# Kernel optimization log

Hardware: AMD Instinct MI355X
Metric: run time of the kernel (lower is better)

## Reference

```python
import jax, jax.numpy as jnp
import numpy as np

METRIC = (1.0, 1.0, 1.0, 1.0, -1.0)  # Cl(4,1) signature
N_HEADS = 8
EPS = 1e-6


def _cayley():
    # Cayley table C[a, b, k]: e_a * e_b = sum_k C[a,b,k] e_k, blades indexed by bitmask over 5 generators.
    C = np.zeros((32, 32, 32), dtype=np.float32)
    for a in range(32):
        for b in range(32):
            s = 0
            t = a >> 1
            while t:
                s += bin(t & b).count('1')
                t >>= 1
            sign = -1.0 if (s & 1) else 1.0
            for i in range(5):
                if (a & b) >> i & 1:
                    sign *= METRIC[i]
            C[a, b, a ^ b] = sign
    return C

_C_NP = _cayley()
GP_MAP = jnp.asarray(_C_NP)  # (32,32,32)
SIG = jnp.asarray(_C_NP[np.arange(32), np.arange(32), 0])  # blade square signs, (32,)


def normalize_cl41(x):
    # normalize each multivector (last-dim 32 blades) to unit RMS
    return x / jnp.sqrt(jnp.mean(x * x, axis=-1, keepdims=True) + EPS)


def versor_linear(x, W):
    # x: (B,S,I,32), W: (O,I,32); out_k = sum_{i,j,l} W[o,i,j] C[j,l,k] x[b,s,i,l]
    O, I, _ = W.shape
    W_op = jnp.einsum('oij,jlk->oilk', W, GP_MAP)  # (O,I,32,32)
    W_mat = W_op.transpose(1, 2, 0, 3).reshape(I * 32, O * 32)
    B, S = x.shape[0], x.shape[1]
    out = (x.reshape(B, S, I * 32) @ W_mat).reshape(B, S, O, 32)
    return normalize_cl41(out)


def versor_attention(x, Wq, Wk, Wv, Wo, lam):
    B, S, D, _ = x.shape
    H = N_HEADS
    hd = D // H

    def split_heads(t):  # (B,S,D,32) -> (B,H,S,hd,32)
        return t.reshape(B, S, H, hd, 32).transpose(0, 2, 1, 3, 4)

    q = split_heads(versor_linear(x, Wq))
    k = split_heads(versor_linear(x, Wk))
    v = split_heads(versor_linear(x, Wv))

    q_flat = (q * SIG).reshape(B, H, S, hd * 32)  # signature-weighted
    k_flat = k.reshape(B, H, S, hd * 32)

    scalar = jnp.einsum('bhsd,bhtd->bhst', q_flat, k_flat)
    scale = 1.0 / jnp.sqrt(jnp.asarray(hd, x.dtype))
    score = scalar * scale

    # torque term: sqrt(relu(|q|^2 |k|^2 - (q.k)^2) + eps) / sqrt(hd)
    q_norm_sq = jnp.sum(q_flat * q_flat, axis=-1)[..., :, None]  # (B,H,S,1)
    k_norm_sq = jnp.sum(k_flat * k_flat, axis=-1)[..., None, :]  # (B,H,1,S)
    torque = jnp.sqrt(jax.nn.relu(q_norm_sq * k_norm_sq - scalar * scalar) + EPS) * scale
    score = score + lam * torque

    probs = jax.nn.softmax(score, axis=-1)
    out = jnp.einsum('bhst,bhtdl->bhsdl', probs, v)  # (B,H,S,hd,32)
    out = out.transpose(0, 2, 1, 3, 4).reshape(B, S, D, 32)
    return versor_linear(out, Wo)


def setup_inputs() -> dict:
    key = jax.random.key(0)
    ks = jax.random.split(key, 5)
    B, S, D = 2, 1024, 128
    std = (2.0 / (D * 32)) ** 0.5  # Versor init
    x = jax.random.normal(ks[0], (B, S, D, 32), jnp.float32)
    Wq = jax.random.normal(ks[1], (D, D, 32), jnp.float32) * std
    Wk = jax.random.normal(ks[2], (D, D, 32), jnp.float32) * std
    Wv = jax.random.normal(ks[3], (D, D, 32), jnp.float32) * std
    Wo = jax.random.normal(ks[4], (D, D, 32), jnp.float32) * std
    attn_lambda = jnp.float32(0.1)
    return {'x': x, 'Wq': Wq, 'Wk': Wk, 'Wv': Wv, 'Wo': Wo, 'attn_lambda': attn_lambda}


def reference(x, Wq, Wk, Wv, Wo, attn_lambda):
    return versor_attention(x, Wq, Wk, Wv, Wo, attn_lambda)
```

## Files before the change

kernel.cpp:

```cpp
#include <hip/hip_runtime.h>
#include <stdint.h>

typedef __attribute__((ext_vector_type(4))) float    f32x4;
typedef __attribute__((ext_vector_type(8))) short    s16x8;
typedef __attribute__((ext_vector_type(4))) short    s16x4;
typedef __attribute__((ext_vector_type(8))) _Float16 f16x8;

#define DEV __device__ __forceinline__

DEV float blade_sign(int a, int b){
    int s = 0, t = a >> 1;
    while (t){ s += __popc(t & b); t >>= 1; }
    float sg = (s & 1) ? -1.0f : 1.0f;
    return ((a & b) & 16) ? -sg : sg;
}
DEV short f2h(float v){
    _Float16 h = (_Float16)v;
    return __builtin_bit_cast(short, h);
}
DEV float h2f(short b){
    return (float)__builtin_bit_cast(_Float16, b);
}
DEV void wait_vm(int n){
    if (n == 12)     asm volatile("s_waitcnt vmcnt(12)" ::: "memory");
    else if (n == 8) asm volatile("s_waitcnt vmcnt(8)" ::: "memory");
    else if (n == 6) asm volatile("s_waitcnt vmcnt(6)" ::: "memory");
    else if (n == 4) asm volatile("s_waitcnt vmcnt(4)" ::: "memory");
    else             asm volatile("s_waitcnt vmcnt(0)" ::: "memory");
}

__global__ __launch_bounds__(256) void cast_f32_f16(const float* __restrict__ in,
                                                    short* __restrict__ out){
    const size_t idx = (size_t)blockIdx.x * 256 + threadIdx.x;
    const float4* p = reinterpret_cast<const float4*>(in) + idx * 2;
    float4 a = p[0], b = p[1];
    s16x8 o;
    o[0]=f2h(a.x); o[1]=f2h(a.y); o[2]=f2h(a.z); o[3]=f2h(a.w);
    o[4]=f2h(b.x); o[5]=f2h(b.y); o[6]=f2h(b.z); o[7]=f2h(b.w);
    *reinterpret_cast<s16x8*>(out + idx * 8) = o;
}

DEV void build_wmat_body(const float* __restrict__ W, short* __restrict__ WmT,
                         int idx){
    const int n  = idx >> 9;
    const int kg = idx & 511;
    const int o = n >> 5, kb = n & 31;
    const int i = kg >> 2, l0 = (kg & 3) * 8;
    const float* wrow = W + (size_t)(o * 128 + i) * 32;
    s16x8 v;
    #pragma unroll
    for (int e = 0; e < 8; ++e){
        const int l = l0 + e, j = kb ^ l;
        v[e] = f2h(wrow[j] * blade_sign(j, l));
    }
    *reinterpret_cast<s16x8*>(WmT + (size_t)n * 4096 + kg * 8) = v;
}

__global__ __launch_bounds__(256) void build_wmat(const float* __restrict__ W,
                                                  short* __restrict__ WmT){
    build_wmat_body(W, WmT, blockIdx.x * 256 + threadIdx.x);
}

__global__ __launch_bounds__(256) void build_wmat3(const float* __restrict__ Wq,
                                                   const float* __restrict__ Wk,
                                                   const float* __restrict__ Wv,
                                                   short* __restrict__ WmT3){
    const int w = blockIdx.y;
    const float* W = (w == 0) ? Wq : ((w == 1) ? Wk : Wv);
    build_wmat_body(W, WmT3 + (size_t)w * 4096 * 4096,
                    blockIdx.x * 256 + threadIdx.x);
}

__global__ __launch_bounds__(256) void row_norms(const short* __restrict__ Q,
                                                 const short* __restrict__ Kq,
                                                 float* __restrict__ Nq,
                                                 float* __restrict__ Nk){
    const int row  = blockIdx.x * 4 + (threadIdx.x >> 6);
    const int lane = threadIdx.x & 63;
    const int b = row >> 13, h = (row >> 10) & 7, s = row & 1023;
    const size_t off = ((size_t)(b * 1024 + s)) * 4096 + h * 512 + lane * 8;
    s16x8 a = *reinterpret_cast<const s16x8*>(Q + off);
    s16x8 c = *reinterpret_cast<const s16x8*>(Kq + off);
    float sq = 0.f, sk = 0.f;
    #pragma unroll
    for (int e = 0; e < 8; ++e){
        float fa = h2f(a[e]); sq = fmaf(fa, fa, sq);
        float fc = h2f(c[e]); sk = fmaf(fc, fc, sk);
    }
    #pragma unroll
    for (int m = 1; m < 64; m <<= 1){
        sq += __shfl_xor(sq, m);
        sk += __shfl_xor(sk, m);
    }
    if (lane == 0){ Nq[row] = sq; Nk[row] = sk; }
}

__global__ __launch_bounds__(256) void softmax_rows(float* __restrict__ Sc){
    const int row  = blockIdx.x * 4 + (threadIdx.x >> 6);
    const int lane = threadIdx.x & 63;
    float* p = Sc + (size_t)row * 1024;
    float v[16];
    float mx = -3.0e38f;
    #pragma unroll
    for (int j = 0; j < 16; ++j){ v[j] = p[lane + j * 64]; mx = fmaxf(mx, v[j]); }
    #pragma unroll
    for (int m = 1; m < 64; m <<= 1) mx = fmaxf(mx, __shfl_xor(mx, m));
    float sum = 0.f;
    #pragma unroll
    for (int j = 0; j < 16; ++j){ v[j] = __expf(v[j] - mx); sum += v[j]; }
    #pragma unroll
    for (int m = 1; m < 64; m <<= 1) sum += __shfl_xor(sum, m);
    const float inv = 1.0f / sum;
    short* pb = reinterpret_cast<short*>(p);
    #pragma unroll
    for (int j = 0; j < 16; ++j) pb[lane + j * 64] = f2h(v[j] * inv);
}

#define GLOAD_LDS(gp, lp) \
    __builtin_amdgcn_global_load_lds( \
        (const __attribute__((address_space(1))) void*)(const void*)(gp), \
        (__attribute__((address_space(3))) void*)(void*)(lp), 16, 0, 0)

#define QKV_TILE(T, WN, PF)                                                     \
  {                                                                             \
    const int bb = cur * 12288;                                                 \
    wait_vm(WN);                                                                \
    __builtin_amdgcn_s_barrier();                                               \
    asm volatile("" ::: "memory");                                              \
    __builtin_amdgcn_sched_barrier(0);                                          \
    const int sb = stg * 12288;                                                 \
    if (PF){                                                                    \
        GLOAD_LDS(gA0 + (size_t)((T) + 2) * 32, lds + sb + dA + 0 * 512);       \
        GLOAD_LDS(gA1 + (size_t)((T) + 2) * 32, lds + sb + dA + 1 * 512);       \
        GLOAD_LDS(gA2 + (size_t)((T) + 2) * 32, lds + sb + dA + 2 * 512);       \
        GLOAD_LDS(gA3 + (size_t)((T) + 2) * 32, lds + sb + dA + 3 * 512);       \
    }                                                                           \
    f16x8 av[4], bv[4];                                                         \
    _Pragma("unroll")                                                           \
    for (int i = 0; i < 4; ++i){                                                \
        av[i] = *reinterpret_cast<const f16x8*>(lds + bb + ard + i * 512);      \
        bv[i] = *reinterpret_cast<const f16x8*>(lds + bb + brd + i * 512);      \
    }                                                                           \
    __builtin_amdgcn_s_setprio(1);                                              \
    _Pragma("unroll")                                                           \
    for (int mi = 0; mi < 4; ++mi)                                              \
        _Pragma("unroll")                                                       \
        for (int ni = 0; ni < 4; ++ni)                                          \
            acc[mi][ni] = __builtin_amdgcn_mfma_f32_16x16x32_f16(               \
                av[mi], bv[ni], acc[mi][ni], 0, 0, 0);                          \
    __builtin_amdgcn_s_setprio(0);                                              \
    if (PF){                                                                    \
        GLOAD_LDS(gB0 + (size_t)((T) + 2) * 32, lds + sb + dB + 0 * 512);       \
        GLOAD_LDS(gB1 + (size_t)((T) + 2) * 32, lds + sb + dB + 1 * 512);       \
    }                                                                           \
    f16x8 aw[4];                                                                \
    _Pragma("unroll")                                                           \
    for (int i = 0; i < 4; ++i)                                                 \
        aw[i] = *reinterpret_cast<const f16x8*>(lds + bb + ard + (4 + i) * 512);\
    __builtin_amdgcn_s_setprio(1);                                              \
    _Pragma("unroll")                                                           \
    for (int mi = 0; mi < 4; ++mi)                                              \
        _Pragma("unroll")                                                       \
        for (int ni = 0; ni < 4; ++ni)                                          \
            acc[4 + mi][ni] = __builtin_amdgcn_mfma_f32_16x16x32_f16(           \
                aw[mi], bv[ni], acc[4 + mi][ni], 0, 0, 0);                      \
    __builtin_amdgcn_s_setprio(0);                                              \
    cur = (cur == 2) ? 0 : cur + 1;                                             \
    stg = (stg == 2) ? 0 : stg + 1;                                             \
  }

__global__ __launch_bounds__(256, 2) void versor_gemm_qkv2(
    const short* __restrict__ Xf,
    const short* __restrict__ WmT3,
    short* __restrict__ OQ,
    short* __restrict__ OK,
    short* __restrict__ OV)
{
    extern __shared__ short lds[];

    const int tid  = threadIdx.x;
    const int lane = tid & 63;
    const int wid  = tid >> 6;
    const int wm   = wid >> 1;
    const int wn   = wid & 1;

    const int wg  = blockIdx.x + blockIdx.y * 96;
    const int xcd = wg & 7;
    const int u   = wg >> 3;
    const int bm  = u & 7;
    const int bn  = xcd * 12 + (u >> 3);
    const int row0 = bm * 256;
    const int col0 = bn * 128;

    const int lda = 4096, ldb = 4096;

    const int jsw = ((lane & 3) ^ ((lane >> 3) & 3)) * 8;
    const short* gA0 = Xf + (size_t)(row0 + wid * 64 + (lane >> 2)) * lda + jsw;
    const short* gA1 = gA0 + (size_t)16 * lda;
    const short* gA2 = gA0 + (size_t)32 * lda;
    const short* gA3 = gA0 + (size_t)48 * lda;
    const short* gB0 = WmT3 + (size_t)(col0 + wid * 32 + (lane >> 2)) * ldb + jsw;
    const short* gB1 = gB0 + (size_t)16 * ldb;
    const int dA = wid * 4 * 512;
    const int dB = 8192 + wid * 2 * 512;

    const int swz = ((lane >> 4) ^ (((lane & 15) >> 1) & 3)) * 8;
    const int ard = (wm * 128 + (lane & 15)) * 32 + swz;
    const int brd = 8192 + (wn * 64 + (lane & 15)) * 32 + swz;

    f32x4 acc[8][4];
    #pragma unroll
    for (int i = 0; i < 8; ++i)
        #pragma unroll
        for (int j = 0; j < 4; ++j)
            acc[i][j] = (f32x4){0.f, 0.f, 0.f, 0.f};

    const int NT = 4096 >> 5;

    #pragma unroll
    for (int pt = 0; pt < 2; ++pt){
        const int sb = pt * 12288;
        GLOAD_LDS(gA0 + pt * 32, lds + sb + dA + 0 * 512);
        GLOAD_LDS(gA1 + pt * 32, lds + sb + dA + 1 * 512);
        GLOAD_LDS(gA2 + pt * 32, lds + sb + dA + 2 * 512);
        GLOAD_LDS(gA3 + pt * 32, lds + sb + dA + 3 * 512);
        GLOAD_LDS(gB0 + pt * 32, lds + sb + dB + 0 * 512);
        GLOAD_LDS(gB1 + pt * 32, lds + sb + dB + 1 * 512);
    }

    int cur = 0, stg = 2;
    for (int t = 0; t < NT - 1; ++t)
        QKV_TILE(t, 6, (t + 2 < NT))
    QKV_TILE(NT - 1, 0, false)

    const int rb = row0 + wm * 128 + (lane >> 4) * 4;

    #pragma unroll
    for (int mi = 0; mi < 8; ++mi){
        #pragma unroll
        for (int g = 0; g < 2; ++g){
            f32x4 a0 = acc[mi][2 * g], a1 = acc[mi][2 * g + 1];
            f32x4 ss = a0 * a0 + a1 * a1;
            #pragma unroll
            for (int m = 1; m < 16; m <<= 1){
                ss.x += __shfl_xor(ss.x, m);
                ss.y += __shfl_xor(ss.y, m);
                ss.z += __shfl_xor(ss.z, m);
                ss.w += __shfl_xor(ss.w, m);
            }
            f32x4 inv;
            inv.x = 1.0f / sqrtf(ss.x * 0.03125f + 1e-6f);
            inv.y = 1.0f / sqrtf(ss.y * 0.03125f + 1e-6f);
            inv.z = 1.0f / sqrtf(ss.z * 0.03125f + 1e-6f);
            inv.w = 1.0f / sqrtf(ss.w * 0.03125f + 1e-6f);
            acc[mi][2 * g]     = a0 * inv;
            acc[mi][2 * g + 1] = a1 * inv;
        }
    }

    const int zsel = col0 >> 12;
    const int cbm  = (col0 & 4095) + wn * 64 + (lane & 15);
    if (zsel == 0){
        const float sg0 = blade_sign(lane & 15, lane & 15);
        const float sg1 = blade_sign(16 | (lane & 15), 16 | (lane & 15));
        #pragma unroll
        for (int mi = 0; mi < 8; ++mi)
            #pragma unroll
            for (int ni = 0; ni < 4; ++ni){
                const f32x4 v = acc[mi][ni] * ((ni & 1) ? sg1 : sg0);
                #pragma unroll
                for (int j = 0; j < 4; ++j)
                    OQ[(size_t)(rb + mi * 16 + j) * 4096 + (cbm + ni * 16)] = f2h(v[j]);
            }
    } else if (zsel == 1){
        #pragma unroll
        for (int mi = 0; mi < 8; ++mi)
            #pragma unroll
            for (int ni = 0; ni < 4; ++ni)
                #pragma unroll
                for (int j = 0; j < 4; ++j)
                    OK[(size_t)(rb + mi * 16 + j) * 4096 + (cbm + ni * 16)] = f2h(acc[mi][ni][j]);
    } else {
        #pragma unroll
        for (int mi = 0; mi < 8; ++mi){
            const int r = rb + mi * 16;
            const int b = r >> 10, tt = r & 1023;
            #pragma unroll
            for (int ni = 0; ni < 4; ++ni){
                const int c = cbm + ni * 16;
                const int h = c >> 9, f = c & 511;
                s16x4 pv;
                #pragma unroll
                for (int j = 0; j < 4; ++j) pv[j] = f2h(acc[mi][ni][j]);
                *reinterpret_cast<s16x4*>(OV + ((size_t)((b * 8 + h) * 512 + f)) * 1024 + tt) = pv;
            }
        }
    }
}

#define R3_TILE(T, WN, PF)                                                      \
  {                                                                             \
    const int bb = cur * 8192;                                                  \
    wait_vm(WN);                                                                \
    __builtin_amdgcn_s_barrier();                                               \
    asm volatile("" ::: "memory");                                              \
    __builtin_amdgcn_sched_barrier(0);                                          \
    const int sb = stg * 8192;                                                  \
    if (PF){                                                                    \
        GLOAD_LDS(gA0 + (size_t)((T) + 2) * 32, lds + sb + dA0);                \
        GLOAD_LDS(gA1 + (size_t)((T) + 2) * 32, lds + sb + dA1);                \
    }                                                                           \
    f16x8 av[4], bv[4];                                                         \
    _Pragma("unroll")                                                           \
    for (int i = 0; i < 4; ++i)                                                 \
        av[i] = *reinterpret_cast<const f16x8*>(lds + bb + ard + i * 512);      \
    bv[0] = *reinterpret_cast<const f16x8*>(lds + bb + brd + 0 * 512);          \
    bv[1] = *reinterpret_cast<const f16x8*>(lds + bb + brd + 1 * 512);          \
    __builtin_amdgcn_s_setprio(1);                                              \
    _Pragma("unroll")                                                           \
    for (int mi = 0; mi < 4; ++mi)                                              \
        _Pragma("unroll")                                                       \
        for (int ni = 0; ni < 2; ++ni)                                          \
            acc[mi][ni] = __builtin_amdgcn_mfma_f32_16x16x32_f16(               \
                av[mi], bv[ni], acc[mi][ni], 0, 0, 0);                          \
    __builtin_amdgcn_s_setprio(0);                                              \
    if (PF){                                                                    \
        GLOAD_LDS(gB0 + (size_t)((T) + 2) * 32, lds + sb + dB0);                \
        GLOAD_LDS(gB1 + (size_t)((T) + 2) * 32, lds + sb + dB1);                \
    }                                                                           \
    bv[2] = *reinterpret_cast<const f16x8*>(lds + bb + brd + 2 * 512);          \
    bv[3] = *reinterpret_cast<const f16x8*>(lds + bb + brd + 3 * 512);          \
    __builtin_amdgcn_s_setprio(1);                                              \
    _Pragma("unroll")                                                           \
    for (int mi = 0; mi < 4; ++mi)                                              \
        _Pragma("unroll")                                                       \
        for (int ni = 2; ni < 4; ++ni)                                          \
            acc[mi][ni] = __builtin_amdgcn_mfma_f32_16x16x32_f16(               \
                av[mi], bv[ni], acc[mi][ni], 0, 0, 0);                          \
    __builtin_amdgcn_s_setprio(0);                                              \
    cur = (cur == 2) ? 0 : cur + 1;                                             \
    stg = (stg == 2) ? 0 : stg + 1;                                             \
  }

template<int EPI, int CPX>
__global__ __launch_bounds__(256, 3) void versor_gemm_r3(
    const short* __restrict__ Abase, int lda,
    const short* __restrict__ Bbase, int ldb,
    int K, void* __restrict__ OutP,
    short* __restrict__ OQ, short* __restrict__ OK, short* __restrict__ OV)
{
    __shared__ short lds[3 * 8192];

    const int tid  = threadIdx.x;
    const int lane = tid & 63;
    const int wid  = tid >> 6;
    const int wr   = wid >> 1;
    const int wc   = wid & 1;
    const int z    = blockIdx.z;

    int bn, bm;
    if constexpr (CPX > 0){
        const int wg  = blockIdx.x + blockIdx.y * gridDim.x;
        const int xcd = wg & 7;
        const int u   = wg >> 3;
        bm = u & 15;
        bn = xcd * CPX + (u >> 4);
    } else {
        bn = blockIdx.x; bm = blockIdx.y;
    }

    const short* A = Abase;
    const short* B = Bbase;
    if constexpr (EPI == 5){
        A += (size_t)z * 1024 * 2048;
        B += (size_t)z * 512 * 1024;
    }
    const int row0 = bm * 128;
    const int col0 = bn * 128;

    const int jsw = ((lane & 3) ^ ((lane >> 3) & 3)) * 8;
    const short* gA0 = A + (size_t)(row0 + wid * 16 + (lane >> 2)) * lda + jsw;
    const short* gA1 = gA0 + (size_t)64 * lda;
    const short* gB0 = B + (size_t)(col0 + wid * 16 + (lane >> 2)) * ldb + jsw;
    const short* gB1 = gB0 + (size_t)64 * ldb;
    const int dA0 = wid * 512,        dA1 = 2048 + wid * 512;
    const int dB0 = 4096 + wid * 512, dB1 = 6144 + wid * 512;

    const int swz = ((lane >> 4) ^ (((lane & 15) >> 1) & 3)) * 8;
    const int ard = (wr * 64 + (lane & 15)) * 32 + swz;
    const int brd = 4096 + (wc * 64 + (lane & 15)) * 32 + swz;

    f32x4 acc[4][4];
    #pragma unroll
    for (int i = 0; i < 4; ++i)
        #pragma unroll
        for (int j = 0; j < 4; ++j)
            acc[i][j] = (f32x4){0.f, 0.f, 0.f, 0.f};

    const int NT = K >> 5;

    #pragma unroll
    for (int pt = 0; pt < 2; ++pt){
        const int sb = pt * 8192;
        GLOAD_LDS(gA0 + pt * 32, lds + sb + dA0);
        GLOAD_LDS(gA1 + pt * 32, lds + sb + dA1);
        GLOAD_LDS(gB0 + pt * 32, lds + sb + dB0);
        GLOAD_LDS(gB1 + pt * 32, lds + sb + dB1);
    }

    int cur = 0, stg = 2;
    for (int t = 0; t < NT - 1; ++t)
        R3_TILE(t, 4, (t + 2 < NT))
    R3_TILE(NT - 1, 0, false)

    const int rb = row0 + wr * 64 + (lane >> 4) * 4;
    const int cb = col0 + wc * 64 + (lane & 15);

    if constexpr (EPI == 3){
        #pragma unroll
        for (int mi = 0; mi < 4; ++mi){
            #pragma unroll
            for (int g = 0; g < 2; ++g){
                f32x4 a0 = acc[mi][2 * g], a1 = acc[mi][2 * g + 1];
                f32x4 ss = a0 * a0 + a1 * a1;
                #pragma unroll
                for (int m = 1; m < 16; m <<= 1){
                    ss.x += __shfl_xor(ss.x, m);
                    ss.y += __shfl_xor(ss.y, m);
                    ss.z += __shfl_xor(ss.z, m);
                    ss.w += __shfl_xor(ss.w, m);
                }
                f32x4 inv;
                inv.x = 1.0f / sqrtf(ss.x * 0.03125f + 1e-6f);
                inv.y = 1.0f / sqrtf(ss.y * 0.03125f + 1e-6f);
                inv.z = 1.0f / sqrtf(ss.z * 0.03125f + 1e-6f);
                inv.w = 1.0f / sqrtf(ss.w * 0.03125f + 1e-6f);
                acc[mi][2 * g]     = a0 * inv;
                acc[mi][2 * g + 1] = a1 * inv;
            }
        }
        float* Of = (float*)OutP;
        #pragma unroll
        for (int mi = 0; mi < 4; ++mi)
            #pragma unroll
            for (int ni = 0; ni < 4; ++ni)
                #pragma unroll
                for (int j = 0; j < 4; ++j)
                    Of[(size_t)(rb + mi * 16 + j) * 4096 + (cb + ni * 16)] = acc[mi][ni][j];
    }
    if constexpr (EPI == 5){
        short* Ob = (short*)OutP;
        const int b = z >> 3, h = z & 7;
        #pragma unroll
        for (int mi = 0; mi < 4; ++mi)
            #pragma unroll
            for (int ni = 0; ni < 4; ++ni)
                #pragma unroll
                for (int j = 0; j < 4; ++j)
                    Ob[(size_t)(b * 1024 + rb + mi * 16 + j) * 4096 + h * 512 + (cb + ni * 16)]
                        = f2h(acc[mi][ni][j]);
    }
    (void)OQ; (void)OK; (void)OV;
}

#define SC_TILE(T, WN, PF)                                                      \
  {                                                                             \
    const int bb = ((T) & 3) * 16384;                                           \
    wait_vm(WN);                                                                \
    __builtin_amdgcn_s_barrier();                                               \
    asm volatile("" ::: "memory");                                              \
    __builtin_amdgcn_sched_barrier(0);                                          \
    if (PF){                                                                    \
        const int nb = (((T) + 3) & 3) * 16384;                                 \
        GLOAD_LDS(gA0 + (size_t)((T) + 3) * 32, lds + nb + dA0);                \
        GLOAD_LDS(gA1 + (size_t)((T) + 3) * 32, lds + nb + dA1);                \
    }                                                                           \
    f16x8 av[4], bv[4];                                                         \
    _Pragma("unroll")                                                           \
    for (int i = 0; i < 4; ++i){                                                \
        av[i] = *reinterpret_cast<const f16x8*>(lds + bb + ard + i * 512);      \
        bv[i] = *reinterpret_cast<const f16x8*>(lds + bb + brd + i * 512);      \
    }                                                                           \
    __builtin_amdgcn_s_setprio(1);                                              \
    _Pragma("unroll")                                                           \
    for (int mi = 0; mi < 4; ++mi)                                              \
        _Pragma("unroll")                                                       \
        for (int ni = 0; ni < 4; ++ni)                                          \
            acc[mi][ni] = __builtin_amdgcn_mfma_f32_16x16x32_f16(               \
                av[mi], bv[ni], acc[mi][ni], 0, 0, 0);                          \
    __builtin_amdgcn_s_setprio(0);                                              \
    if (PF){                                                                    \
        const int nb = (((T) + 3) & 3) * 16384;                                 \
        GLOAD_LDS(gB0 + (size_t)((T) + 3) * 32, lds + nb + dB0);                \
        GLOAD_LDS(gB1 + (size_t)((T) + 3) * 32, lds + nb + dB1);                \
    }                                                                           \
    f16x8 aw[4];                                                                \
    _Pragma("unroll")                                                           \
    for (int i = 0; i < 4; ++i)                                                 \
        aw[i] = *reinterpret_cast<const f16x8*>(lds + bb + ard + (4 + i) * 512);\
    __builtin_amdgcn_s_setprio(1);                                              \
    _Pragma("unroll")                                                           \
    for (int mi = 0; mi < 4; ++mi)                                              \
        _Pragma("unroll")                                                       \
        for (int ni = 0; ni < 4; ++ni)                                          \
            acc[4 + mi][ni] = __builtin_amdgcn_mfma_f32_16x16x32_f16(           \
                aw[mi], bv[ni], acc[4 + mi][ni], 0, 0, 0);                      \
    __builtin_amdgcn_s_setprio(0);                                              \
  }

__global__ __launch_bounds__(512, 2) void versor_gemm_sc(
    const short* __restrict__ Qbase, const short* __restrict__ Kbase,
    int K, float* __restrict__ OutP,
    const float* __restrict__ NqP, const float* __restrict__ NkP,
    const float* __restrict__ LamP)
{
    extern __shared__ short lds[];

    const int tid  = threadIdx.x;
    const int lane = tid & 63;
    const int wid  = tid >> 6;
    const int wm   = wid >> 2;
    const int wn   = wid & 3;
    const int z    = blockIdx.z;

    const int b = z >> 3, h = z & 7;
    const size_t off = (size_t)b * 1024 * 4096 + (size_t)h * 512;
    const short* A = Qbase + off;
    const short* B = Kbase + off;
    const int lda = 4096, ldb = 4096;
    const int row0 = blockIdx.y * 256;
    const int col0 = blockIdx.x * 256;

    const int jsw = ((lane & 3) ^ ((lane >> 3) & 3)) * 8;
    const short* gA0 = A + (size_t)(row0 + wid * 32 + (lane >> 2)) * lda + jsw;
    const short* gA1 = gA0 + (size_t)16 * lda;
    const short* gB0 = B + (size_t)(col0 + wid * 32 + (lane >> 2)) * ldb + jsw;
    const short* gB1 = gB0 + (size_t)16 * ldb;
    const int dA0 = wid * 1024, dA1 = dA0 + 512;
    const int dB0 = 8192 + wid * 1024, dB1 = dB0 + 512;

    const int swz = ((lane >> 4) ^ (((lane & 15) >> 1) & 3)) * 8;
    const int ard = (wm * 128 + (lane & 15)) * 32 + swz;
    const int brd = 8192 + (wn * 64 + (lane & 15)) * 32 + swz;

    f32x4 acc[8][4];
    #pragma unroll
    for (int i = 0; i < 8; ++i)
        #pragma unroll
        for (int j = 0; j < 4; ++j)
            acc[i][j] = (f32x4){0.f, 0.f, 0.f, 0.f};

    const int NT = K >> 5;

    #pragma unroll
    for (int pt = 0; pt < 3; ++pt){
        const int bb = pt * 16384;
        GLOAD_LDS(gA0 + pt * 32, lds + bb + dA0);
        GLOAD_LDS(gA1 + pt * 32, lds + bb + dA1);
        GLOAD_LDS(gB0 + pt * 32, lds + bb + dB0);
        GLOAD_LDS(gB1 + pt * 32, lds + bb + dB1);
    }

    for (int t = 0; t < NT - 2; ++t)
        SC_TILE(t, 8, (t + 3 < NT))
    SC_TILE(NT - 2, 4, false)
    SC_TILE(NT - 1, 0, false)

    const int rb = row0 + wm * 128 + (lane >> 4) * 4;
    const int cb = col0 + wn * 64 + (lane & 15);

    float* Of = OutP + (size_t)z * 1024 * 1024;
    const float lam = *LamP;
    const float* nq = NqP + z * 1024;
    const float* nk = NkP + z * 1024;
    #pragma unroll
    for (int mi = 0; mi < 8; ++mi)
        #pragma unroll
        for (int j = 0; j < 4; ++j){
            const int r = rb + mi * 16 + j;
            const float qn = nq[r];
            #pragma unroll
            for (int ni = 0; ni < 4; ++ni){
                const int c = cb + ni * 16;
                const float sc = acc[mi][ni][j];
                const float tq = sqrtf(fmaxf(qn * nk[c] - sc * sc, 0.0f) + 1e-6f);
                Of[(size_t)r * 1024 + c] = 0.25f * (sc + lam * tq);
            }
        }
}

extern "C" void kernel_launch(void* const* d_in, const int* in_sizes, int n_in,
                              void* d_out, int out_size, void* d_ws, size_t ws_size,
                              hipStream_t stream)
{
    (void)in_sizes; (void)n_in; (void)out_size; (void)ws_size;
    const float* x   = (const float*)d_in[0];
    const float* Wq  = (const float*)d_in[1];
    const float* Wk  = (const float*)d_in[2];
    const float* Wv  = (const float*)d_in[3];
    const float* Wo  = (const float*)d_in[4];
    const float* lam = (const float*)d_in[5];
    float* out = (float*)d_out;
    char*  ws  = (char*)d_ws;

    short* Xf   = (short*)(ws);
    short* WmT3 = (short*)(ws + (16u  << 20));
    short* Qf   = (short*)(ws + (112u << 20));
    short* Kf   = (short*)(ws + (128u << 20));
    short* Vt   = (short*)(ws + (144u << 20));
    float* Nq   = (float*)(ws + (160u << 20));
    float* Nk   = (float*)(ws + (160u << 20) + (64u << 10));
    float* Sc   = (float*)(ws + (16u  << 20));
    short* WmTo = (short*)(ws + (80u  << 20));
    short* Attn = Xf;

    const int SC_LDS  = 131072;
    const int QKV_LDS = 73728;
    hipFuncSetAttribute(reinterpret_cast<const void*>(versor_gemm_sc),
                        hipFuncAttributeMaxDynamicSharedMemorySize, SC_LDS);
    hipFuncSetAttribute(reinterpret_cast<const void*>(versor_gemm_qkv2),
                        hipFuncAttributeMaxDynamicSharedMemorySize, QKV_LDS);

    dim3 blk(256), blk8(512);
    cast_f32_f16<<<4096, blk, 0, stream>>>(x, Xf);

    dim3 gw3(8192, 3);
    build_wmat3<<<gw3, blk, 0, stream>>>(Wq, Wk, Wv, WmT3);

    dim3 gqkv(96, 8, 1);
    versor_gemm_qkv2<<<gqkv, blk, QKV_LDS, stream>>>(Xf, WmT3, Qf, Kf, Vt);

    row_norms<<<4096, blk, 0, stream>>>(Qf, Kf, Nq, Nk);

    build_wmat<<<8192, blk, 0, stream>>>(Wo, WmTo);

    dim3 gsc(4, 4, 16);
    versor_gemm_sc<<<gsc, blk8, SC_LDS, stream>>>(Qf, Kf, 512, Sc, Nq, Nk, lam);
    softmax_rows<<<4096, blk, 0, stream>>>(Sc);

    dim3 gpv(4, 8, 16);
    versor_gemm_r3<5, 0><<<gpv, blk, 0, stream>>>(
        (const short*)Sc, 2048, Vt, 1024, 1024, Attn, nullptr, nullptr, nullptr);

    dim3 gfin(32, 16, 1);
    versor_gemm_r3<3, 4><<<gfin, blk, 0, stream>>>(
        Attn, 4096, WmTo, 4096, 4096, out, nullptr, nullptr, nullptr);
}
```

Measured before the change: 525.7 us.

## Restructure QKV GEMM: B operand direct to registers, A via LDS double buffer

The QKV projection GEMM now loads its weight (B) fragments straight from global memory into registers, ping-ponging between two register sets. Only the activation (A) tile is staged in LDS, double-buffered with a K-step of 64 instead of a triple-buffered K-step of 32. The aim is to halve the number of barriers per K, cut LDS traffic and footprint (static 64KB), and overlap global loads with MFMA work. The cost is higher register pressure and B reads that are not shared across waves sharing the same columns, which means more L2 traffic. Unused OQ/OK/OV parameters are also removed from versor_gemm_r3.

```diff
diff --git a/kernel.cpp b/kernel.cpp
--- a/kernel.cpp
+++ b/kernel.cpp
@@ -22,9 +22,8 @@
     return (float)__builtin_bit_cast(_Float16, b);
 }
 DEV void wait_vm(int n){
-    if (n == 12)     asm volatile("s_waitcnt vmcnt(12)" ::: "memory");
+    if (n == 16)     asm volatile("s_waitcnt vmcnt(16)" ::: "memory");
     else if (n == 8) asm volatile("s_waitcnt vmcnt(8)" ::: "memory");
-    else if (n == 6) asm volatile("s_waitcnt vmcnt(6)" ::: "memory");
     else if (n == 4) asm volatile("s_waitcnt vmcnt(4)" ::: "memory");
     else             asm volatile("s_waitcnt vmcnt(0)" ::: "memory");
 }
@@ -121,62 +120,55 @@
         (const __attribute__((address_space(1))) void*)(const void*)(gp), \
         (__attribute__((address_space(3))) void*)(void*)(lp), 16, 0, 0)
 
-#define QKV_TILE(T, WN, PF)                                                     \
-  {                                                                             \
-    const int bb = cur * 12288;                                                 \
-    wait_vm(WN);                                                                \
+#define Q3_ISSUE_B(SET, T)                                                      \
+    _Pragma("unroll")                                                           \
+    for (int ni = 0; ni < 4; ++ni){                                             \
+        SET[ni][0] = *reinterpret_cast<const f16x8*>(gB + ni * 65536 + (size_t)(T) * 64);      \
+        SET[ni][1] = *reinterpret_cast<const f16x8*>(gB + ni * 65536 + (size_t)(T) * 64 + 32); \
+    }
+
+#define Q3_ISSUE_A(BUF, T)                                                      \
+    _Pragma("unroll")                                                           \
+    for (int g = 0; g < 8; ++g)                                                 \
+        GLOAD_LDS(gA + (size_t)g * 131072 + (size_t)(T) * 64,                   \
+                  lds + (BUF) * 16384 + g * 2048 + wid * 512);
+
+#define Q3_COMPUTE(SET, BUF)                                                    \
+  { const short* ab = lds + (BUF) * 16384 + ard;                                \
+    _Pragma("unroll")                                                           \
+    for (int p = 0; p < 4; ++p){                                                \
+        f16x8 a0k0 = *reinterpret_cast<const f16x8*>(ab + (2*p)*1024   + okk0); \
+        f16x8 a0k1 = *reinterpret_cast<const f16x8*>(ab + (2*p)*1024   + okk1); \
+        f16x8 a1k0 = *reinterpret_cast<const f16x8*>(ab + (2*p+1)*1024 + okk0); \
+        f16x8 a1k1 = *reinterpret_cast<const f16x8*>(ab + (2*p+1)*1024 + okk1); \
+        __builtin_amdgcn_s_setprio(1);                                          \
+        _Pragma("unroll")                                                       \
+        for (int ni = 0; ni < 4; ++ni){                                         \
+            acc[2*p][ni]   = __builtin_amdgcn_mfma_f32_16x16x32_f16(            \
+                a0k0, SET[ni][0], acc[2*p][ni], 0, 0, 0);                       \
+            acc[2*p][ni]   = __builtin_amdgcn_mfma_f32_16x16x32_f16(            \
+                a0k1, SET[ni][1], acc[2*p][ni], 0, 0, 0);                       \
+            acc[2*p+1][ni] = __builtin_amdgcn_mfma_f32_16x16x32_f16(            \
+                a1k0, SET[ni][0], acc[2*p+1][ni], 0, 0, 0);                     \
+            acc[2*p+1][ni] = __builtin_amdgcn_mfma_f32_16x16x32_f16(            \
+                a1k1, SET[ni][1], acc[2*p+1][ni], 0, 0, 0);                     \
+        }                                                                       \
+        __builtin_amdgcn_s_setprio(0);                                          \
+    } }
+
+#define Q3_SYNC()                                                               \
     __builtin_amdgcn_s_barrier();                                               \
     asm volatile("" ::: "memory");                                              \
-    __builtin_amdgcn_sched_barrier(0);                                          \
-    const int sb = stg * 12288;                                                 \
-    if (PF){                                                                    \
-        GLOAD_LDS(gA0 + (size_t)((T) + 2) * 32, lds + sb + dA + 0 * 512);       \
-        GLOAD_LDS(gA1 + (size_t)((T) + 2) * 32, lds + sb + dA + 1 * 512);       \
-        GLOAD_LDS(gA2 + (size_t)((T) + 2) * 32, lds + sb + dA + 2 * 512);       \
-        GLOAD_LDS(gA3 + (size_t)((T) + 2) * 32, lds + sb + dA + 3 * 512);       \
-    }                                                                           \
-    f16x8 av[4], bv[4];                                                         \
-    _Pragma("unroll")                                                           \
-    for (int i = 0; i < 4; ++i){                                                \
-        av[i] = *reinterpret_cast<const f16x8*>(lds + bb + ard + i * 512);      \
-        bv[i] = *reinterpret_cast<const f16x8*>(lds + bb + brd + i * 512);      \
-    }                                                                           \
-    __builtin_amdgcn_s_setprio(1);                                              \
-    _Pragma("unroll")                                                           \
-    for (int mi = 0; mi < 4; ++mi)                                              \
-        _Pragma("unroll")                                                       \
-        for (int ni = 0; ni < 4; ++ni)                                          \
-            acc[mi][ni] = __builtin_amdgcn_mfma_f32_16x16x32_f16(               \
-                av[mi], bv[ni], acc[mi][ni], 0, 0, 0);                          \
-    __builtin_amdgcn_s_setprio(0);                                              \
-    if (PF){                                                                    \
-        GLOAD_LDS(gB0 + (size_t)((T) + 2) * 32, lds + sb + dB + 0 * 512);       \
-        GLOAD_LDS(gB1 + (size_t)((T) + 2) * 32, lds + sb + dB + 1 * 512);       \
-    }                                                                           \
-    f16x8 aw[4];                                                                \
-    _Pragma("unroll")                                                           \
-    for (int i = 0; i < 4; ++i)                                                 \
-        aw[i] = *reinterpret_cast<const f16x8*>(lds + bb + ard + (4 + i) * 512);\
-    __builtin_amdgcn_s_setprio(1);                                              \
-    _Pragma("unroll")                                                           \
-    for (int mi = 0; mi < 4; ++mi)                                              \
-        _Pragma("unroll")                                                       \
-        for (int ni = 0; ni < 4; ++ni)                                          \
-            acc[4 + mi][ni] = __builtin_amdgcn_mfma_f32_16x16x32_f16(           \
-                aw[mi], bv[ni], acc[4 + mi][ni], 0, 0, 0);                      \
-    __builtin_amdgcn_s_setprio(0);                                              \
-    cur = (cur == 2) ? 0 : cur + 1;                                             \
-    stg = (stg == 2) ? 0 : stg + 1;                                             \
-  }
-
-__global__ __launch_bounds__(256, 2) void versor_gemm_qkv2(
+    __builtin_amdgcn_sched_barrier(0);
+
+__global__ __launch_bounds__(256, 2) void versor_gemm_qkv3(
     const short* __restrict__ Xf,
     const short* __restrict__ WmT3,
     short* __restrict__ OQ,
     short* __restrict__ OK,
     short* __restrict__ OV)
 {
-    extern __shared__ short lds[];
+    __shared__ short lds[2 * 16384];
 
     const int tid  = threadIdx.x;
     const int lane = tid & 63;
@@ -191,22 +183,17 @@
     const int bn  = xcd * 12 + (u >> 3);
     const int row0 = bm * 256;
     const int col0 = bn * 128;
-
     const int lda = 4096, ldb = 4096;
 
-    const int jsw = ((lane & 3) ^ ((lane >> 3) & 3)) * 8;
-    const short* gA0 = Xf + (size_t)(row0 + wid * 64 + (lane >> 2)) * lda + jsw;
-    const short* gA1 = gA0 + (size_t)16 * lda;
-    const short* gA2 = gA0 + (size_t)32 * lda;
-    const short* gA3 = gA0 + (size_t)48 * lda;
-    const short* gB0 = WmT3 + (size_t)(col0 + wid * 32 + (lane >> 2)) * ldb + jsw;
-    const short* gB1 = gB0 + (size_t)16 * ldb;
-    const int dA = wid * 4 * 512;
-    const int dB = 8192 + wid * 2 * 512;
-
-    const int swz = ((lane >> 4) ^ (((lane & 15) >> 1) & 3)) * 8;
-    const int ard = (wm * 128 + (lane & 15)) * 32 + swz;
-    const int brd = 8192 + (wn * 64 + (lane & 15)) * 32 + swz;
+    const int jswA = ((lane & 7) ^ ((lane >> 3) & 7)) * 8;
+    const short* gA = Xf + (size_t)(row0 + wid * 8 + (lane >> 3)) * lda + jswA;
+
+    const short* gB = WmT3 + (size_t)(col0 + wn * 64 + (lane & 15)) * ldb + (lane >> 4) * 8;
+
+    const int l4 = lane >> 4;
+    const int okk0 = ((((lane >> 2) & 1) << 2)       | (l4 ^ (lane & 3))) * 8;
+    const int okk1 = (((1 ^ ((lane >> 2) & 1)) << 2) | (l4 ^ (lane & 3))) * 8;
+    const int ard  = (wm * 128 + (lane & 15)) * 64;
 
     f32x4 acc[8][4];
     #pragma unroll
@@ -215,23 +202,32 @@
         for (int j = 0; j < 4; ++j)
             acc[i][j] = (f32x4){0.f, 0.f, 0.f, 0.f};
 
-    const int NT = 4096 >> 5;
-
-    #pragma unroll
-    for (int pt = 0; pt < 2; ++pt){
-        const int sb = pt * 12288;
-        GLOAD_LDS(gA0 + pt * 32, lds + sb + dA + 0 * 512);
-        GLOAD_LDS(gA1 + pt * 32, lds + sb + dA + 1 * 512);
-        GLOAD_LDS(gA2 + pt * 32, lds + sb + dA + 2 * 512);
-        GLOAD_LDS(gA3 + pt * 32, lds + sb + dA + 3 * 512);
-        GLOAD_LDS(gB0 + pt * 32, lds + sb + dB + 0 * 512);
-        GLOAD_LDS(gB1 + pt * 32, lds + sb + dB + 1 * 512);
-    }
-
-    int cur = 0, stg = 2;
-    for (int t = 0; t < NT - 1; ++t)
-        QKV_TILE(t, 6, (t + 2 < NT))
-    QKV_TILE(NT - 1, 0, false)
+    f16x8 bX[4][2], bY[4][2];
+    const int NT = 64;
+
+    Q3_ISSUE_B(bX, 0)
+    Q3_ISSUE_A(0, 0)
+
+    for (int t = 0; t < NT; t += 2){
+        Q3_SYNC()
+        if (t + 1 < NT){
+            Q3_ISSUE_B(bY, t + 1)
+            Q3_ISSUE_A(1, t + 1)
+            wait_vm(16);
+        } else {
+            wait_vm(0);
+        }
+        Q3_COMPUTE(bX, 0)
+        Q3_SYNC()
+        if (t + 2 < NT){
+            Q3_ISSUE_B(bX, t + 2)
+            Q3_ISSUE_A(0, t + 2)
+            wait_vm(16);
+        } else {
+            wait_vm(0);
+        }
+        Q3_COMPUTE(bY, 1)
+    }
 
     const int rb = row0 + wm * 128 + (lane >> 4) * 4;
 
@@ -346,8 +342,7 @@
 __global__ __launch_bounds__(256, 3) void versor_gemm_r3(
     const short* __restrict__ Abase, int lda,
     const short* __restrict__ Bbase, int ldb,
-    int K, void* __restrict__ OutP,
-    short* __restrict__ OQ, short* __restrict__ OK, short* __restrict__ OV)
+    int K, void* __restrict__ OutP)
 {
     __shared__ short lds[3 * 8192];
 
@@ -460,7 +455,6 @@
                     Ob[(size_t)(b * 1024 + rb + mi * 16 + j) * 4096 + h * 512 + (cb + ni * 16)]
                         = f2h(acc[mi][ni][j]);
     }
-    (void)OQ; (void)OK; (void)OV;
 }
 
 #define SC_TILE(T, WN, PF)                                                      \
@@ -614,12 +608,9 @@
     short* WmTo = (short*)(ws + (80u  << 20));
     short* Attn = Xf;
 
-    const int SC_LDS  = 131072;
-    const int QKV_LDS = 73728;
+    const int SC_LDS = 131072;
     hipFuncSetAttribute(reinterpret_cast<const void*>(versor_gemm_sc),
                         hipFuncAttributeMaxDynamicSharedMemorySize, SC_LDS);
-    hipFuncSetAttribute(reinterpret_cast<const void*>(versor_gemm_qkv2),
-                        hipFuncAttributeMaxDynamicSharedMemorySize, QKV_LDS);
 
     dim3 blk(256), blk8(512);
     cast_f32_f16<<<4096, blk, 0, stream>>>(x, Xf);
@@ -628,7 +619,7 @@
     build_wmat3<<<gw3, blk, 0, stream>>>(Wq, Wk, Wv, WmT3);
 
     dim3 gqkv(96, 8, 1);
-    versor_gemm_qkv2<<<gqkv, blk, QKV_LDS, stream>>>(Xf, WmT3, Qf, Kf, Vt);
+    versor_gemm_qkv3<<<gqkv, blk, 0, stream>>>(Xf, WmT3, Qf, Kf, Vt);
 
     row_norms<<<4096, blk, 0, stream>>>(Qf, Kf, Nq, Nk);
 
@@ -640,9 +631,9 @@
 
     dim3 gpv(4, 8, 16);
     versor_gemm_r3<5, 0><<<gpv, blk, 0, stream>>>(
-        (const short*)Sc, 2048, Vt, 1024, 1024, Attn, nullptr, nullptr, nullptr);
+        (const short*)Sc, 2048, Vt, 1024, 1024, Attn);
 
     dim3 gfin(32, 16, 1);
     versor_gemm_r3<3, 4><<<gfin, blk, 0, stream>>>(
-        Attn, 4096, WmTo, 4096, 4096, out, nullptr, nullptr, nullptr);
-}
+        Attn, 4096, WmTo, 4096, 4096, out);
+}
```

New measurement: 597.3 us. 1.14x slower.

## Switch QKV GEMM to double-buffered static LDS with higher occupancy

Applied to the files above, without the earlier changes.

Replaces the triple-buffered LDS pipeline of the QKV projection GEMM with a two-buffer scheme using static shared memory, and raises the launch bound to three blocks per CU. Prefetch of tile t+2 now happens after a second barrier at the end of each iteration. This aims to fit more workgroups per CU to hide latency, at the cost of an extra barrier per tile and possible register pressure with 128 accumulator values per thread. Unused pointer parameters are also removed from another GEMM kernel.

```diff
diff --git a/kernel.cpp b/kernel.cpp
--- a/kernel.cpp
+++ b/kernel.cpp
@@ -22,8 +22,7 @@
     return (float)__builtin_bit_cast(_Float16, b);
 }
 DEV void wait_vm(int n){
-    if (n == 12)     asm volatile("s_waitcnt vmcnt(12)" ::: "memory");
-    else if (n == 8) asm volatile("s_waitcnt vmcnt(8)" ::: "memory");
+    if (n == 8)      asm volatile("s_waitcnt vmcnt(8)" ::: "memory");
     else if (n == 6) asm volatile("s_waitcnt vmcnt(6)" ::: "memory");
     else if (n == 4) asm volatile("s_waitcnt vmcnt(4)" ::: "memory");
     else             asm volatile("s_waitcnt vmcnt(0)" ::: "memory");
@@ -121,62 +120,25 @@
         (const __attribute__((address_space(1))) void*)(const void*)(gp), \
         (__attribute__((address_space(3))) void*)(void*)(lp), 16, 0, 0)
 
-#define QKV_TILE(T, WN, PF)                                                     \
+#define QKV_STAGE(BUF, T)                                                       \
   {                                                                             \
-    const int bb = cur * 12288;                                                 \
-    wait_vm(WN);                                                                \
-    __builtin_amdgcn_s_barrier();                                               \
-    asm volatile("" ::: "memory");                                              \
-    __builtin_amdgcn_sched_barrier(0);                                          \
-    const int sb = stg * 12288;                                                 \
-    if (PF){                                                                    \
-        GLOAD_LDS(gA0 + (size_t)((T) + 2) * 32, lds + sb + dA + 0 * 512);       \
-        GLOAD_LDS(gA1 + (size_t)((T) + 2) * 32, lds + sb + dA + 1 * 512);       \
-        GLOAD_LDS(gA2 + (size_t)((T) + 2) * 32, lds + sb + dA + 2 * 512);       \
-        GLOAD_LDS(gA3 + (size_t)((T) + 2) * 32, lds + sb + dA + 3 * 512);       \
-    }                                                                           \
-    f16x8 av[4], bv[4];                                                         \
-    _Pragma("unroll")                                                           \
-    for (int i = 0; i < 4; ++i){                                                \
-        av[i] = *reinterpret_cast<const f16x8*>(lds + bb + ard + i * 512);      \
-        bv[i] = *reinterpret_cast<const f16x8*>(lds + bb + brd + i * 512);      \
-    }                                                                           \
-    __builtin_amdgcn_s_setprio(1);                                              \
-    _Pragma("unroll")                                                           \
-    for (int mi = 0; mi < 4; ++mi)                                              \
-        _Pragma("unroll")                                                       \
-        for (int ni = 0; ni < 4; ++ni)                                          \
-            acc[mi][ni] = __builtin_amdgcn_mfma_f32_16x16x32_f16(               \
-                av[mi], bv[ni], acc[mi][ni], 0, 0, 0);                          \
-    __builtin_amdgcn_s_setprio(0);                                              \
-    if (PF){                                                                    \
-        GLOAD_LDS(gB0 + (size_t)((T) + 2) * 32, lds + sb + dB + 0 * 512);       \
-        GLOAD_LDS(gB1 + (size_t)((T) + 2) * 32, lds + sb + dB + 1 * 512);       \
-    }                                                                           \
-    f16x8 aw[4];                                                                \
-    _Pragma("unroll")                                                           \
-    for (int i = 0; i < 4; ++i)                                                 \
-        aw[i] = *reinterpret_cast<const f16x8*>(lds + bb + ard + (4 + i) * 512);\
-    __builtin_amdgcn_s_setprio(1);                                              \
-    _Pragma("unroll")                                                           \
-    for (int mi = 0; mi < 4; ++mi)                                              \
-        _Pragma("unroll")                                                       \
-        for (int ni = 0; ni < 4; ++ni)                                          \
-            acc[4 + mi][ni] = __builtin_amdgcn_mfma_f32_16x16x32_f16(           \
-                aw[mi], bv[ni], acc[4 + mi][ni], 0, 0, 0);                      \
-    __builtin_amdgcn_s_setprio(0);                                              \
-    cur = (cur == 2) ? 0 : cur + 1;                                             \
-    stg = (stg == 2) ? 0 : stg + 1;                                             \
+    const int sb = (BUF) * 12288;                                               \
+    GLOAD_LDS(gA0 + (size_t)(T) * 32, lds + sb + dA + 0 * 512);                 \
+    GLOAD_LDS(gA1 + (size_t)(T) * 32, lds + sb + dA + 1 * 512);                 \
+    GLOAD_LDS(gA2 + (size_t)(T) * 32, lds + sb + dA + 2 * 512);                 \
+    GLOAD_LDS(gA3 + (size_t)(T) * 32, lds + sb + dA + 3 * 512);                 \
+    GLOAD_LDS(gB0 + (size_t)(T) * 32, lds + sb + dB + 0 * 512);                 \
+    GLOAD_LDS(gB1 + (size_t)(T) * 32, lds + sb + dB + 1 * 512);                 \
   }
 
-__global__ __launch_bounds__(256, 2) void versor_gemm_qkv2(
+__global__ __launch_bounds__(256, 3) void versor_gemm_qkv4(
     const short* __restrict__ Xf,
     const short* __restrict__ WmT3,
     short* __restrict__ OQ,
     short* __restrict__ OK,
     short* __restrict__ OV)
 {
-    extern __shared__ short lds[];
+    __shared__ short lds[2 * 12288];
 
     const int tid  = threadIdx.x;
     const int lane = tid & 63;
@@ -191,7 +153,6 @@
     const int bn  = xcd * 12 + (u >> 3);
     const int row0 = bm * 256;
     const int col0 = bn * 128;
-
     const int lda = 4096, ldb = 4096;
 
     const int jsw = ((lane & 3) ^ ((lane >> 3) & 3)) * 8;
@@ -217,21 +178,51 @@
 
     const int NT = 4096 >> 5;
 
-    #pragma unroll
-    for (int pt = 0; pt < 2; ++pt){
-        const int sb = pt * 12288;
-        GLOAD_LDS(gA0 + pt * 32, lds + sb + dA + 0 * 512);
-        GLOAD_LDS(gA1 + pt * 32, lds + sb + dA + 1 * 512);
-        GLOAD_LDS(gA2 + pt * 32, lds + sb + dA + 2 * 512);
-        GLOAD_LDS(gA3 + pt * 32, lds + sb + dA + 3 * 512);
-        GLOAD_LDS(gB0 + pt * 32, lds + sb + dB + 0 * 512);
-        GLOAD_LDS(gB1 + pt * 32, lds + sb + dB + 1 * 512);
-    }
-
-    int cur = 0, stg = 2;
-    for (int t = 0; t < NT - 1; ++t)
-        QKV_TILE(t, 6, (t + 2 < NT))
-    QKV_TILE(NT - 1, 0, false)
+    QKV_STAGE(0, 0)
+    QKV_STAGE(1, 1)
+
+    for (int t = 0; t < NT; ++t){
+        if (t + 1 < NT) wait_vm(6);
+        else            wait_vm(0);
+        __builtin_amdgcn_s_barrier();
+        asm volatile("" ::: "memory");
+        __builtin_amdgcn_sched_barrier(0);
+
+        const int bb = (t & 1) * 12288;
+        f16x8 av[4], bv[4];
+        #pragma unroll
+        for (int i = 0; i < 4; ++i){
+            av[i] = *reinterpret_cast<const f16x8*>(lds + bb + ard + i * 512);
+            bv[i] = *reinterpret_cast<const f16x8*>(lds + bb + brd + i * 512);
+        }
+        __builtin_amdgcn_s_setprio(1);
+        #pragma unroll
+        for (int mi = 0; mi < 4; ++mi)
+            #pragma unroll
+            for (int ni = 0; ni < 4; ++ni)
+                acc[mi][ni] = __builtin_amdgcn_mfma_f32_16x16x32_f16(
+                    av[mi], bv[ni], acc[mi][ni], 0, 0, 0);
+        __builtin_amdgcn_s_setprio(0);
+
+        f16x8 aw[4];
+        #pragma unroll
+        for (int i = 0; i < 4; ++i)
+            aw[i] = *reinterpret_cast<const f16x8*>(lds + bb + ard + (4 + i) * 512);
+        __builtin_amdgcn_s_setprio(1);
+        #pragma unroll
+        for (int mi = 0; mi < 4; ++mi)
+            #pragma unroll
+            for (int ni = 0; ni < 4; ++ni)
+                acc[4 + mi][ni] = __builtin_amdgcn_mfma_f32_16x16x32_f16(
+                    aw[mi], bv[ni], acc[4 + mi][ni], 0, 0, 0);
+        __builtin_amdgcn_s_setprio(0);
+
+        __builtin_amdgcn_s_barrier();
+        asm volatile("" ::: "memory");
+        __builtin_amdgcn_sched_barrier(0);
+        if (t + 2 < NT)
+            QKV_STAGE(t & 1, t + 2)
+    }
 
     const int rb = row0 + wm * 128 + (lane >> 4) * 4;
 
@@ -346,8 +337,7 @@
 __global__ __launch_bounds__(256, 3) void versor_gemm_r3(
     const short* __restrict__ Abase, int lda,
     const short* __restrict__ Bbase, int ldb,
-    int K, void* __restrict__ OutP,
-    short* __restrict__ OQ, short* __restrict__ OK, short* __restrict__ OV)
+    int K, void* __restrict__ OutP)
 {
     __shared__ short lds[3 * 8192];
 
@@ -460,7 +450,6 @@
                     Ob[(size_t)(b * 1024 + rb + mi * 16 + j) * 4096 + h * 512 + (cb + ni * 16)]
                         = f2h(acc[mi][ni][j]);
     }
-    (void)OQ; (void)OK; (void)OV;
 }
 
 #define SC_TILE(T, WN, PF)                                                      \
@@ -614,12 +603,9 @@
     short* WmTo = (short*)(ws + (80u  << 20));
     short* Attn = Xf;
 
-    const int SC_LDS  = 131072;
-    const int QKV_LDS = 73728;
+    const int SC_LDS = 131072;
     hipFuncSetAttribute(reinterpret_cast<const void*>(versor_gemm_sc),
                         hipFuncAttributeMaxDynamicSharedMemorySize, SC_LDS);
-    hipFuncSetAttribute(reinterpret_cast<const void*>(versor_gemm_qkv2),
-                        hipFuncAttributeMaxDynamicSharedMemorySize, QKV_LDS);
 
     dim3 blk(256), blk8(512);
     cast_f32_f16<<<4096, blk, 0, stream>>>(x, Xf);
@@ -628,7 +614,7 @@
     build_wmat3<<<gw3, blk, 0, stream>>>(Wq, Wk, Wv, WmT3);
 
     dim3 gqkv(96, 8, 1);
-    versor_gemm_qkv2<<<gqkv, blk, QKV_LDS, stream>>>(Xf, WmT3, Qf, Kf, Vt);
+    versor_gemm_qkv4<<<gqkv, blk, 0, stream>>>(Xf, WmT3, Qf, Kf, Vt);
 
     row_norms<<<4096, blk, 0, stream>>>(Qf, Kf, Nq, Nk);
 
@@ -640,9 +626,9 @@
 
     dim3 gpv(4, 8, 16);
     versor_gemm_r3<5, 0><<<gpv, blk, 0, stream>>>(
-        (const short*)Sc, 2048, Vt, 1024, 1024, Attn, nullptr, nullptr, nullptr);
+        (const short*)Sc, 2048, Vt, 1024, 1024, Attn);
 
     dim3 gfin(32, 16, 1);
     versor_gemm_r3<3, 4><<<gfin, blk, 0, stream>>>(
-        Attn, 4096, WmTo, 4096, 4096, out, nullptr, nullptr, nullptr);
-}
+        Attn, 4096, WmTo, 4096, 4096, out);
+}
```

New measurement: 528.5 us. About the same (+0.5%).
